# Kernel optimization log

Measured on AMD Instinct MI355X. Metric: run time of the kernel, lower is better.

## Reference

```python
import jax, jax.numpy as jnp
import numpy as np

D_MODEL = 256
NUM_HEADS = 4
D_HEAD = D_MODEL // NUM_HEADS
LN_EPS = 1e-5
NEG_INF = -1e9


def setup_inputs() -> dict:
    key = jax.random.key(0)
    ks = jax.random.split(key, 8)
    B, N = 4, 2048
    s = 1.0 / np.sqrt(D_MODEL)
    return {
        "x": jax.random.normal(ks[0], (B, N, D_MODEL), dtype=jnp.float32),
        "Wq": jax.random.normal(ks[1], (D_MODEL, D_MODEL), dtype=jnp.float32) * s,
        "Wk": jax.random.normal(ks[2], (D_MODEL, D_MODEL), dtype=jnp.float32) * s,
        "Wv": jax.random.normal(ks[3], (D_MODEL, D_MODEL), dtype=jnp.float32) * s,
        "Wo": jax.random.normal(ks[4], (D_MODEL, D_MODEL), dtype=jnp.float32) * s,
        "bo": jnp.zeros((D_MODEL,), dtype=jnp.float32),
        "gamma": jnp.ones((D_MODEL,), dtype=jnp.float32),
        "beta": jnp.zeros((D_MODEL,), dtype=jnp.float32),
        "k_neighbors": 8,
    }


def build_knn_adj(x, k):
    # x: [B, N, D]; returns symmetric 0/1 adjacency [B, N, N]
    B, N, _ = x.shape
    xn = x / jnp.maximum(jnp.linalg.norm(x, axis=-1, keepdims=True), 1e-12)
    sim = jnp.einsum('bnd,bmd->bnm', xn, xn)  # [B, N, N]
    _, idx = jax.lax.top_k(sim, k + 1)        # [B, N, k+1]
    b = jnp.arange(B)[:, None, None]
    r = jnp.arange(N)[None, :, None]
    adj = jnp.zeros((B, N, N), dtype=jnp.float32).at[b, r, idx].add(1.0)
    adj = jnp.maximum(adj, jnp.swapaxes(adj, 1, 2))
    return adj


def layer_norm(x, gamma, beta):
    mu = jnp.mean(x, axis=-1, keepdims=True)
    var = jnp.mean(jnp.square(x - mu), axis=-1, keepdims=True)
    return (x - mu) * jax.lax.rsqrt(var + LN_EPS) * gamma + beta


def reference(x, Wq, Wk, Wv, Wo, bo, gamma, beta, k_neighbors):
    B, N, D = x.shape
    adj = build_knn_adj(x, k_neighbors)  # [B, N, N]

    def split_heads(t):  # [B, N, D] -> [B, H, N, d]
        return jnp.transpose(t.reshape(B, N, NUM_HEADS, D_HEAD), (0, 2, 1, 3))

    q = split_heads(x @ Wq)
    k = split_heads(x @ Wk)
    v = split_heads(x @ Wv)

    scores = jnp.einsum('bhnd,bhmd->bhnm', q, k) / jnp.sqrt(jnp.float32(D_HEAD))
    scores = jnp.where(adj[:, None, :, :] > 0, scores, NEG_INF)
    attn = jax.nn.softmax(scores, axis=-1)  # dropout is identity at inference
    out = jnp.einsum('bhnm,bhmd->bhnd', attn, v)
    out = jnp.transpose(out, (0, 2, 1, 3)).reshape(B, N, D)
    out = out @ Wo + bo
    return layer_norm(x + out, gamma, beta)
```

## Files before the change

kernel.cpp:

```cpp
#include <hip/hip_runtime.h>
#include <hip/hip_bf16.h>
#include <math.h>

#define BATCH 4
#define N 2048
#define D 256
#define NH 4
#define DH 64
#define TOPK 9
#define NEG_BIG -1e30f

typedef __bf16 bf16;
typedef __bf16 bf16x4 __attribute__((ext_vector_type(4)));
typedef __bf16 bf16x8 __attribute__((ext_vector_type(8)));
typedef float f32x4 __attribute__((ext_vector_type(4)));

#define PK3(a,b,c) ((a) | ((b) << 2) | ((c) << 4))
#define PK6(a,b,c,d,e,f) ((a) | ((b) << 2) | ((c) << 4) | ((d) << 6) | ((e) << 8) | ((f) << 10))

#define WAITVM(Nc) __builtin_amdgcn_s_waitcnt((((Nc) & 0xf)) | (7u << 4) | (0xfu << 8) | ((((unsigned)(Nc)) >> 4) << 14))

__device__ __forceinline__ void async_cp16(const bf16* g, const bf16* l) {
  __builtin_amdgcn_global_load_lds(
      (const __attribute__((address_space(1))) void*)(uintptr_t)g,
      (__attribute__((address_space(3))) void*)(uintptr_t)l, 16, 0, 0);
}

__global__ __launch_bounds__(64) void prep_kernel(const float* __restrict__ x,
                                                  const float* __restrict__ Wq,
                                                  const float* __restrict__ Wk,
                                                  const float* __restrict__ Wv,
                                                  const float* __restrict__ Wo,
                                                  bf16* __restrict__ XsN,
                                                  bf16* __restrict__ Wt,
                                                  float* __restrict__ norms,
                                                  uint4* __restrict__ mask4) {
  int blk = blockIdx.x;
  int lane = threadIdx.x;
  if (blk < 8192) {
    float4 v = *(const float4*)(x + (size_t)blk * D + lane * 4);
    float ss = v.x * v.x + v.y * v.y + v.z * v.z + v.w * v.w;
    for (int off = 32; off; off >>= 1) ss += __shfl_down(ss, off);
    ss = __shfl(ss, 0);
    float nrm = fmaxf(sqrtf(ss), 1e-12f);
    if (lane == 0) norms[blk] = nrm;
    float sc = 1.0f / nrm;
    float xs[4] = {v.x * sc, v.y * sc, v.z * sc, v.w * sc};
    bf16* o = XsN + (size_t)blk * 512 + lane * 4;
#pragma unroll
    for (int j = 0; j < 4; ++j) {
      float xv = xs[j];
      bf16 h = (bf16)xv;
      o[j] = h;
      o[256 + j] = (bf16)(xv - (float)h);
    }
  } else if (blk < 9216) {
    int jj = blk - 8192;
    const float* W = (jj < 256) ? Wq : (jj < 512) ? Wk : (jj < 768) ? Wv : Wo;
    int j = jj & 255;
    bf16* dst = Wt + (size_t)jj * 512;
    for (int k = lane; k < 256; k += 64) {
      float w = W[(size_t)k * D + j];
      bf16 h = (bf16)w;
      dst[k] = h;
      dst[256 + k] = (bf16)(w - (float)h);
    }
  } else {
    int base = (blk - 9216) * 1024 + lane;
#pragma unroll
    for (int t = 0; t < 16; ++t)
      mask4[base + t * 64] = make_uint4(0, 0, 0, 0);
  }
}

__device__ __forceinline__ void gemm_core128x256(bf16* As, bf16* Bs,
                                                 const bf16* __restrict__ Ab,
                                                 const bf16* __restrict__ Bb,
                                                 void* __restrict__ Cvoid,
                                                 int ldc, int nsteps,
                                                 int amap, int bmap,
                                                 int row0, int col0,
                                                 int outmode, bool mirror,
                                                 const float* __restrict__ rowscale) {
  int tid = threadIdx.x;
  int lane = tid & 63;
  int wv = tid >> 6;
  int wm = (wv >> 1) * 64;
  int wn = (wv & 1) * 128;
  int fr = lane & 15;
  int G = lane >> 4;

  f32x4 acc[4][8] = {};

  auto issue = [&](int st, int buf) {
    int ch = st >> 3;
    int aoff = (((amap >> (ch * 2)) & 3) << 8) | ((st & 7) << 5);
    int boff = (((bmap >> (ch * 2)) & 3) << 8) | ((st & 7) << 5);
#pragma unroll
    for (int q = 0; q < 2; ++q) {
      int s = q * 256 + tid;
      int r = s >> 2, sl = s & 3;
      async_cp16(Ab + (size_t)r * 512 + ((sl ^ ((r >> 1) & 3)) << 3) + aoff,
                 &As[buf * 4096 + s * 8]);
    }
#pragma unroll
    for (int q = 0; q < 4; ++q) {
      int s = q * 256 + tid;
      int r = s >> 2, sl = s & 3;
      async_cp16(Bb + (size_t)r * 512 + ((sl ^ ((r >> 1) & 3)) << 3) + boff,
                 &Bs[buf * 8192 + s * 8]);
    }
  };

  issue(0, 0);
  for (int st = 0; st < nsteps; ++st) {
    int buf = st & 1;
    if (st + 1 < nsteps) {
      issue(st + 1, buf ^ 1);
      WAITVM(6);
    } else {
      WAITVM(0);
    }
    __builtin_amdgcn_s_barrier();
    bf16x8 af[4], bfr[8];
#pragma unroll
    for (int mi = 0; mi < 4; ++mi) {
      int r = wm + mi * 16 + fr;
      af[mi] = *(const bf16x8*)&As[buf * 4096 + r * 32 + ((G ^ ((r >> 1) & 3)) << 3)];
    }
#pragma unroll
    for (int nj = 0; nj < 8; ++nj) {
      int r = wn + nj * 16 + fr;
      bfr[nj] = *(const bf16x8*)&Bs[buf * 8192 + r * 32 + ((G ^ ((r >> 1) & 3)) << 3)];
    }
    __builtin_amdgcn_s_setprio(1);
#pragma unroll
    for (int mi = 0; mi < 4; ++mi)
#pragma unroll
      for (int nj = 0; nj < 8; ++nj)
        acc[mi][nj] = __builtin_amdgcn_mfma_f32_16x16x32_bf16(af[mi], bfr[nj], acc[mi][nj], 0, 0, 0);
    __builtin_amdgcn_s_setprio(0);
    __builtin_amdgcn_s_barrier();
  }

  int er = (lane >> 4) * 4;
  int ec = lane & 15;
#pragma unroll
  for (int mi = 0; mi < 4; ++mi) {
    int rb = row0 + wm + mi * 16 + er;
    float scl[4] = {1.f, 1.f, 1.f, 1.f};
    if (rowscale) {
      float4 s4 = *(const float4*)(rowscale + rb);
      scl[0] = s4.x; scl[1] = s4.y; scl[2] = s4.z; scl[3] = s4.w;
    }
#pragma unroll
    for (int nj = 0; nj < 8; ++nj) {
      int cb = col0 + wn + nj * 16 + ec;
      if (outmode == 1) {
        float* Cb = (float*)Cvoid;
#pragma unroll
        for (int reg = 0; reg < 4; ++reg)
          __builtin_nontemporal_store(acc[mi][nj][reg],
                                      &Cb[(size_t)(rb + reg) * ldc + cb]);
        if (mirror) {
          __builtin_nontemporal_store(acc[mi][nj],
                                      (f32x4*)&Cb[(size_t)cb * ldc + rb]);
        }
      } else {
        bf16* Cb = (bf16*)Cvoid;
#pragma unroll
        for (int reg = 0; reg < 4; ++reg)
          Cb[(size_t)(rb + reg) * ldc + cb] = (bf16)(acc[mi][nj][reg] * scl[reg]);
      }
    }
  }
}

__global__ __launch_bounds__(256, 2) void gemm_fused128x256_kernel(
    const bf16* __restrict__ XsN, float* __restrict__ sim,
    int amap_s, int bmap_s,
    const bf16* __restrict__ Wt, bf16* __restrict__ qkv,
    int amap_q, int bmap_q, const float* __restrict__ norms) {
  __shared__ bf16 As[2 * 128 * 32];
  __shared__ bf16 Bs[2 * 256 * 32];
  int g = blockIdx.x;
  if (g < 288) {
    int xcd = g & 7;
    int z = xcd >> 1;
    int t = (xcd & 1) * 36 + (g >> 3);
    int half = t & 1;
    int u = t >> 1;
    int by = 0;
    while (u >= 8 - by) { u -= 8 - by; ++by; }
    int bx = by + u;
    int row0 = by * 256 + half * 128;
    int col0 = bx * 256;
    gemm_core128x256(As, Bs,
                     XsN + (size_t)z * N * 512 + (size_t)row0 * 512,
                     XsN + (size_t)z * N * 512 + (size_t)col0 * 512,
                     sim + (size_t)z * N * N,
                     N, 24, amap_s, bmap_s, row0, col0,
                     1, bx != by, nullptr);
  } else {
    int t = g - 288;
    int xcd = t & 7;
    int slot = t >> 3;
    int z = xcd >> 1;
    int by = z * 16 + (xcd & 1) * 8 + slot / 3;
    int bx = slot % 3;
    gemm_core128x256(As, Bs,
                     XsN + (size_t)by * 128 * 512,
                     Wt + (size_t)bx * 256 * 512,
                     qkv, 768, 16, amap_q, bmap_q,
                     by * 128, bx * 256, 2, false, norms);
  }
}

__device__ __forceinline__ void gemm_core(bf16* As, bf16* Bs,
                                          const bf16* __restrict__ Ab,
                                          const bf16* __restrict__ Bb,
                                          void* __restrict__ Cvoid,
                                          int lda, int ldb, int ldc,
                                          int nsteps, int amap, int bmap,
                                          int row0, int col0,
                                          int outmode, bool mirror,
                                          const float* __restrict__ rowscale) {
  int tid = threadIdx.x;
  int lane = tid & 63;
  int wv = tid >> 6;
  int wm = (wv >> 1) * 64;
  int wn = (wv & 1) * 64;

  int rbase = tid >> 2;
  int gperm = (tid & 3) ^ ((rbase >> 1) & 3);
  const bf16* ga0 = Ab + (size_t)rbase * lda + gperm * 8;
  const bf16* gb0 = Bb + (size_t)rbase * ldb + gperm * 8;
  int ldsoff = tid * 8;

  int fr = lane & 15;
  int G = lane >> 4;

  f32x4 acc[4][4] = {};

  auto issue = [&](int st, int buf) {
    int ch = st >> 3;
    int aoff = (((amap >> (ch * 2)) & 3) << 8) | ((st & 7) << 5);
    int boff = (((bmap >> (ch * 2)) & 3) << 8) | ((st & 7) << 5);
#pragma unroll
    for (int q = 0; q < 2; ++q)
      async_cp16(ga0 + (size_t)q * 64 * lda + aoff, &As[buf * 4096 + ldsoff + q * 2048]);
#pragma unroll
    for (int q = 0; q < 2; ++q)
      async_cp16(gb0 + (size_t)q * 64 * ldb + boff, &Bs[buf * 4096 + ldsoff + q * 2048]);
  };

  issue(0, 0);
  for (int st = 0; st < nsteps; ++st) {
    int buf = st & 1;
    if (st + 1 < nsteps) {
      issue(st + 1, buf ^ 1);
      WAITVM(4);
    } else {
      WAITVM(0);
    }
    __builtin_amdgcn_s_barrier();
    bf16x8 af[4], bfr[4];
#pragma unroll
    for (int mi = 0; mi < 4; ++mi) {
      int r = wm + mi * 16 + fr;
      af[mi] = *(const bf16x8*)&As[buf * 4096 + r * 32 + ((G ^ ((r >> 1) & 3)) << 3)];
    }
#pragma unroll
    for (int nj = 0; nj < 4; ++nj) {
      int r = wn + nj * 16 + fr;
      bfr[nj] = *(const bf16x8*)&Bs[buf * 4096 + r * 32 + ((G ^ ((r >> 1) & 3)) << 3)];
    }
#pragma unroll
    for (int mi = 0; mi < 4; ++mi)
#pragma unroll
      for (int nj = 0; nj < 4; ++nj)
        acc[mi][nj] = __builtin_amdgcn_mfma_f32_16x16x32_bf16(af[mi], bfr[nj], acc[mi][nj], 0, 0, 0);
    __builtin_amdgcn_s_barrier();
  }

  int er = (lane >> 4) * 4;
  int ec = lane & 15;
#pragma unroll
  for (int mi = 0; mi < 4; ++mi) {
    int rb = row0 + wm + mi * 16 + er;
    float scl[4] = {1.f, 1.f, 1.f, 1.f};
    if (rowscale) {
      float4 s4 = *(const float4*)(rowscale + rb);
      scl[0] = s4.x; scl[1] = s4.y; scl[2] = s4.z; scl[3] = s4.w;
    }
#pragma unroll
    for (int nj = 0; nj < 4; ++nj) {
      int cb = col0 + wn + nj * 16 + ec;
      if (outmode == 1) {
        float* Cb = (float*)Cvoid;
#pragma unroll
        for (int reg = 0; reg < 4; ++reg)
          __builtin_nontemporal_store(acc[mi][nj][reg],
                                      &Cb[(size_t)(rb + reg) * ldc + cb]);
        if (mirror) {
#pragma unroll
          for (int reg = 0; reg < 4; ++reg)
            __builtin_nontemporal_store(acc[mi][nj][reg],
                                        &Cb[(size_t)cb * ldc + rb + reg]);
        }
      } else {
        bf16* Cb = (bf16*)Cvoid;
#pragma unroll
        for (int reg = 0; reg < 4; ++reg)
          Cb[(size_t)(rb + reg) * ldc + cb] = (bf16)(acc[mi][nj][reg] * scl[reg]);
      }
    }
  }
}

__global__ __launch_bounds__(256, 4) void gemm_sim_kernel(const bf16* __restrict__ XsN,
                                                          float* __restrict__ sim,
                                                          int amap, int bmap) {
  __shared__ bf16 As[2 * 128 * 32];
  __shared__ bf16 Bs[2 * 128 * 32];
  int g = blockIdx.x;
  int xcd = g & 7;
  int slot = g >> 3;
  int z = xcd >> 1;
  int t = (xcd & 1) * 68 + slot;
  int by = 0;
  while (t >= 16 - by) { t -= 16 - by; ++by; }
  int bx = by + t;
  gemm_core(As, Bs,
            XsN + (size_t)z * N * 512 + (size_t)by * 128 * 512,
            XsN + (size_t)z * N * 512 + (size_t)bx * 128 * 512,
            sim + (size_t)z * N * N,
            512, 512, N, 24, amap, bmap, by * 128, bx * 128,
            1, bx != by, nullptr);
}

__global__ __launch_bounds__(256, 4) void gemm_qkv_kernel(const bf16* __restrict__ XsN,
                                                          const bf16* __restrict__ Wt,
                                                          bf16* __restrict__ qkv,
                                                          int amap, int bmap,
                                                          const float* __restrict__ norms) {
  __shared__ bf16 As[2 * 128 * 32];
  __shared__ bf16 Bs[2 * 128 * 32];
  gemm_core(As, Bs,
            XsN + (size_t)blockIdx.y * 128 * 512,
            Wt + (size_t)blockIdx.x * 128 * 512,
            qkv, 512, 512, 768, 16, amap, bmap,
            blockIdx.y * 128, blockIdx.x * 128, 2, false, norms);
}

__global__ __launch_bounds__(64) void topk_adj_kernel(const float* __restrict__ sim,
                                                      unsigned* __restrict__ mask) {
  int row = blockIdx.x;
  int lane = threadIdx.x;
  int b = row >> 11, r = row & 2047;
  const float* srow = sim + (size_t)row * N;
  float v[32];
#pragma unroll
  for (int it = 0; it < 8; ++it) {
    float4 q = *(const float4*)(srow + it * 256 + lane * 4);
    v[it * 4 + 0] = q.x; v[it * 4 + 1] = q.y;
    v[it * 4 + 2] = q.z; v[it * 4 + 3] = q.w;
  }
  unsigned removed = 0;
  for (int rs = 0; rs < TOPK; ++rs) {
    float m = -3e38f;
    int mi = 0;
#pragma unroll
    for (int i = 0; i < 32; ++i) {
      float vv = ((removed >> i) & 1u) ? -3e38f : v[i];
      if (vv > m) { m = vv; mi = i; }
    }
    int gidx = ((mi >> 2) << 8) + lane * 4 + (mi & 3);
    for (int off = 32; off; off >>= 1) {
      float om = __shfl_down(m, off);
      int og = __shfl_down(gidx, off);
      if (om > m || (om == m && og < gidx)) { m = om; gidx = og; }
    }
    gidx = __shfl(gidx, 0);
    if (((gidx >> 2) & 63) == lane)
      removed |= 1u << (((gidx >> 8) << 2) | (gidx & 3));
    if (lane == 0) {
      atomicOr(&mask[(size_t)row * 64 + (gidx >> 5)], 1u << (gidx & 31));
      atomicOr(&mask[(((size_t)b << 11) + gidx) * 64 + (r >> 5)], 1u << (r & 31));
    }
  }
}

__global__ __launch_bounds__(256) void attn_kernel(const bf16* __restrict__ qkv,
                                                   const unsigned* __restrict__ mask,
                                                   bf16* __restrict__ aos) {
  __shared__ float sq[4][256];
  __shared__ unsigned short nbr[4][2048];
  __shared__ int s_nn[4];
  int wv = threadIdx.x >> 6;
  int lane = threadIdx.x & 63;
  int g = blockIdx.x;
  int xcd = g & 7;
  int b = xcd >> 1;
  int tile = (xcd & 1) * 256 + (g >> 3);
  int bn = b * N + tile * 4 + wv;
  if (lane == 0) s_nn[wv] = 0;
  {
    bf16x4 qv = *(const bf16x4*)(qkv + (size_t)bn * 768 + lane * 4);
#pragma unroll
    for (int j = 0; j < 4; ++j) sq[wv][lane * 4 + j] = (float)qv[j];
  }
  __syncthreads();
  unsigned bits = mask[(size_t)bn * (N / 32) + lane];
  while (bits) {
    int bit = __ffs(bits) - 1;
    bits &= bits - 1;
    int p = atomicAdd(&s_nn[wv], 1);
    nbr[wv][p] = (unsigned short)(lane * 32 + bit);
  }
  __syncthreads();
  int nn = s_nn[wv];
  const bf16* base = qkv + (size_t)b * N * 768;
  float acc[4] = {0.f, 0.f, 0.f, 0.f};

  auto score4 = [&](int j, float* s) {
    const bf16* kr = base + (size_t)j * 768 + 256;
#pragma unroll
    for (int h = 0; h < 4; ++h) {
      float a = 0.f;
#pragma unroll
      for (int c = 0; c < DH; c += 8) {
        bf16x8 kk = *(const bf16x8*)(kr + h * DH + c);
#pragma unroll
        for (int t = 0; t < 8; ++t) a += sq[wv][h * DH + c + t] * (float)kk[t];
      }
      s[h] = a * 0.125f;
    }
  };

  if (nn <= 64) {
    float s[4] = {NEG_BIG, NEG_BIG, NEG_BIG, NEG_BIG};
    if (lane < nn) score4(nbr[wv][lane], s);
    float w[4], l[4];
#pragma unroll
    for (int h = 0; h < 4; ++h) {
      float m = s[h];
      for (int off = 32; off; off >>= 1) m = fmaxf(m, __shfl_down(m, off));
      m = __shfl(m, 0);
      float e = (lane < nn) ? __expf(s[h] - m) : 0.f;
      float ls = e;
      for (int off = 32; off; off >>= 1) ls += __shfl_down(ls, off);
      l[h] = __shfl(ls, 0);
      w[h] = e;
    }
    int i = 0;
    for (; i + 4 <= nn; i += 4) {
      int j0 = nbr[wv][i + 0], j1 = nbr[wv][i + 1];
      int j2 = nbr[wv][i + 2], j3 = nbr[wv][i + 3];
      const bf16* p0 = base + (size_t)j0 * 768 + 512;
      const bf16* p1 = base + (size_t)j1 * 768 + 512;
      const bf16* p2 = base + (size_t)j2 * 768 + 512;
      const bf16* p3 = base + (size_t)j3 * 768 + 512;
#pragma unroll
      for (int h = 0; h < 4; ++h) {
        acc[h] += __shfl(w[h], i + 0) * (float)p0[h * DH + lane] +
                  __shfl(w[h], i + 1) * (float)p1[h * DH + lane] +
                  __shfl(w[h], i + 2) * (float)p2[h * DH + lane] +
                  __shfl(w[h], i + 3) * (float)p3[h * DH + lane];
      }
    }
    for (; i < nn; ++i) {
      const bf16* p0 = base + (size_t)nbr[wv][i] * 768 + 512;
#pragma unroll
      for (int h = 0; h < 4; ++h) acc[h] += __shfl(w[h], i) * (float)p0[h * DH + lane];
    }
#pragma unroll
    for (int h = 0; h < 4; ++h) acc[h] /= l[h];
  } else {
    float m[4] = {NEG_BIG, NEG_BIG, NEG_BIG, NEG_BIG};
    for (int i0 = 0; i0 < nn; i0 += 64) {
      float s[4] = {NEG_BIG, NEG_BIG, NEG_BIG, NEG_BIG};
      if (i0 + lane < nn) score4(nbr[wv][i0 + lane], s);
#pragma unroll
      for (int h = 0; h < 4; ++h) m[h] = fmaxf(m[h], s[h]);
    }
#pragma unroll
    for (int h = 0; h < 4; ++h) {
      for (int off = 32; off; off >>= 1) m[h] = fmaxf(m[h], __shfl_down(m[h], off));
      m[h] = __shfl(m[h], 0);
    }
    float l[4] = {0.f, 0.f, 0.f, 0.f};
    for (int i0 = 0; i0 < nn; i0 += 64) {
      float s[4] = {NEG_BIG, NEG_BIG, NEG_BIG, NEG_BIG};
      if (i0 + lane < nn) score4(nbr[wv][i0 + lane], s);
      float e[4];
#pragma unroll
      for (int h = 0; h < 4; ++h) {
        e[h] = (i0 + lane < nn) ? __expf(s[h] - m[h]) : 0.f;
        float ls = e[h];
        for (int off = 32; off; off >>= 1) ls += __shfl_down(ls, off);
        l[h] += __shfl(ls, 0);
      }
      int lim = min(64, nn - i0);
      for (int ii = 0; ii < lim; ++ii) {
        const bf16* p0 = base + (size_t)nbr[wv][i0 + ii] * 768 + 512;
#pragma unroll
        for (int h = 0; h < 4; ++h) acc[h] += __shfl(e[h], ii) * (float)p0[h * DH + lane];
      }
    }
#pragma unroll
    for (int h = 0; h < 4; ++h) acc[h] /= l[h];
  }
#pragma unroll
  for (int h = 0; h < 4; ++h) {
    float a = acc[h];
    bf16 hi = (bf16)a;
    aos[(size_t)bn * 512 + h * DH + lane] = hi;
    aos[(size_t)bn * 512 + 256 + h * DH + lane] = (bf16)(a - (float)hi);
  }
}

__global__ __launch_bounds__(256) void projln_kernel(const bf16* __restrict__ A,
                                                     const bf16* __restrict__ Bw,
                                                     const float* __restrict__ x,
                                                     const float* __restrict__ bo,
                                                     const float* __restrict__ gamma,
                                                     const float* __restrict__ beta,
                                                     float* __restrict__ out) {
  __shared__ bf16 As[2 * 32 * 32];
  __shared__ bf16 Bs[2 * 256 * 32];
  __shared__ float rsum[32][4];
  __shared__ float rsq[32][4];
  int tid = threadIdx.x;
  int lane = tid & 63;
  int wv = tid >> 6;
  int wn = wv * 64;
  int row0 = blockIdx.x * 32;

  int rt = tid >> 2;
  int ra = tid >> 2;
  int gpa = (tid & 3) ^ ((ra >> 1) & 3);
  const bf16* ga0 = A + (size_t)(row0 + ra) * 512 + gpa * 8;

  int fr = lane & 15;
  int G = lane >> 4;

  f32x4 acc[2][4] = {};

  auto issue = [&](int st, int buf) {
    int aoff = ((st >> 3) << 8) | ((st & 7) << 5);
    int boff = (st & 7) << 5;
    if (tid < 128)
      async_cp16(ga0 + aoff, &As[buf * 1024 + tid * 8]);
#pragma unroll
    for (int q = 0; q < 4; ++q) {
      int rb = q * 64 + rt;
      int gpb = (tid & 3) ^ ((rb >> 1) & 3);
      async_cp16(Bw + (size_t)rb * 512 + gpb * 8 + boff,
                 &Bs[buf * 8192 + (q * 256 + tid) * 8]);
    }
  };

  issue(0, 0);
  for (int st = 0; st < 16; ++st) {
    int buf = st & 1;
    if (st + 1 < 16) {
      issue(st + 1, buf ^ 1);
      WAITVM(4);
    } else {
      WAITVM(0);
    }
    __builtin_amdgcn_s_barrier();
    bf16x8 af[2], bfr[4];
#pragma unroll
    for (int mi = 0; mi < 2; ++mi) {
      int r = mi * 16 + fr;
      af[mi] = *(const bf16x8*)&As[buf * 1024 + r * 32 + ((G ^ ((r >> 1) & 3)) << 3)];
    }
#pragma unroll
    for (int nj = 0; nj < 4; ++nj) {
      int r = wn + nj * 16 + fr;
      bfr[nj] = *(const bf16x8*)&Bs[buf * 8192 + r * 32 + ((G ^ ((r >> 1) & 3)) << 3)];
    }
#pragma unroll
    for (int mi = 0; mi < 2; ++mi)
#pragma unroll
      for (int nj = 0; nj < 4; ++nj)
        acc[mi][nj] = __builtin_amdgcn_mfma_f32_16x16x32_bf16(af[mi], bfr[nj], acc[mi][nj], 0, 0, 0);
    __builtin_amdgcn_s_barrier();
  }

  int er = (lane >> 4) * 4;
  int ec = lane & 15;
  float bo_c[4], ga_c[4], be_c[4];
#pragma unroll
  for (int nj = 0; nj < 4; ++nj) {
    int c = wn + nj * 16 + ec;
    bo_c[nj] = bo[c]; ga_c[nj] = gamma[c]; be_c[nj] = beta[c];
  }
#pragma unroll
  for (int mi = 0; mi < 2; ++mi)
#pragma unroll
    for (int reg = 0; reg < 4; ++reg) {
      int rloc = mi * 16 + er + reg;
      const float* xr = x + (size_t)(row0 + rloc) * D;
      float su = 0.f, s2 = 0.f;
#pragma unroll
      for (int nj = 0; nj < 4; ++nj) {
        float u = acc[mi][nj][reg] + bo_c[nj] + xr[wn + nj * 16 + ec];
        su += u; s2 += u * u;
      }
#pragma unroll
      for (int m = 1; m <= 8; m <<= 1) {
        su += __shfl_xor(su, m);
        s2 += __shfl_xor(s2, m);
      }
      if (ec == 0) { rsum[rloc][wv] = su; rsq[rloc][wv] = s2; }
    }
  __syncthreads();
#pragma unroll
  for (int mi = 0; mi < 2; ++mi)
#pragma unroll
    for (int reg = 0; reg < 4; ++reg) {
      int rloc = mi * 16 + er + reg;
      float s = rsum[rloc][0] + rsum[rloc][1] + rsum[rloc][2] + rsum[rloc][3];
      float q2 = rsq[rloc][0] + rsq[rloc][1] + rsq[rloc][2] + rsq[rloc][3];
      float mean = s * (1.0f / D);
      float var = q2 * (1.0f / D) - mean * mean;
      float rstd = rsqrtf(var + 1e-5f);
      const float* xr = x + (size_t)(row0 + rloc) * D;
      float* orow = out + (size_t)(row0 + rloc) * D;
#pragma unroll
      for (int nj = 0; nj < 4; ++nj) {
        float u = acc[mi][nj][reg] + bo_c[nj] + xr[wn + nj * 16 + ec];
        orow[wn + nj * 16 + ec] = (u - mean) * rstd * ga_c[nj] + be_c[nj];
      }
    }
}

extern "C" void kernel_launch(void* const* d_in, const int* in_sizes, int n_in,
                              void* d_out, int out_size, void* d_ws, size_t ws_size,
                              hipStream_t stream) {
  const float* x     = (const float*)d_in[0];
  const float* Wq    = (const float*)d_in[1];
  const float* Wk    = (const float*)d_in[2];
  const float* Wv    = (const float*)d_in[3];
  const float* Wo    = (const float*)d_in[4];
  const float* bo    = (const float*)d_in[5];
  const float* gamma = (const float*)d_in[6];
  const float* beta  = (const float*)d_in[7];
  float* out = (float*)d_out;

  char* ws = (char*)d_ws;
  bf16* XsN      = (bf16*)(ws);
  float* sim     = (float*)(ws + 12582912);
  float* norms   = (float*)(ws + 79691776);
  unsigned* mask = (unsigned*)(ws + 79986688);
  bf16* Wt       = (bf16*)(ws + 82083840);

  bool big = ws_size >= (size_t)125000000;
  bf16* qkv = (bf16*)(ws + (big ? 83132416 : 12582912));
  bf16* aos = (bf16*)(ws + (big ? 95715328 : 37748736));

  const int AMAP_SIM = PK6(0, 0, 1, 0, 0, 0);
  const int BMAP_SIM = PK6(0, 1, 0, 0, 0, 0);
  const int AMAP_2T  = PK3(0, 1, 0);
  const int BMAP_2T  = PK3(0, 0, 1);

  prep_kernel<<<9344, 64, 0, stream>>>(x, Wq, Wk, Wv, Wo, XsN, Wt, norms,
                                       (uint4*)mask);

  if (big) {
    gemm_fused128x256_kernel<<<480, 256, 0, stream>>>(
        XsN, sim, AMAP_SIM, BMAP_SIM, Wt, qkv, AMAP_2T, BMAP_2T, norms);
    topk_adj_kernel<<<BATCH * N, 64, 0, stream>>>(sim, mask);
  } else {
    gemm_sim_kernel<<<544, 256, 0, stream>>>(XsN, sim, AMAP_SIM, BMAP_SIM);
    topk_adj_kernel<<<BATCH * N, 64, 0, stream>>>(sim, mask);
    gemm_qkv_kernel<<<dim3(6, 64), 256, 0, stream>>>(XsN, Wt, qkv,
                                                     AMAP_2T, BMAP_2T, norms);
  }

  attn_kernel<<<(BATCH * N) / 4, 256, 0, stream>>>(qkv, mask, aos);

  projln_kernel<<<256, 256, 0, stream>>>(aos, Wt + (size_t)768 * 512,
                                         x, bo, gamma, beta, out);
}
```

Baseline: 187.8 us.

## Fuse per-tile top-k candidate selection into similarity GEMM epilogue

```diff
diff --git a/kernel.cpp b/kernel.cpp
--- a/kernel.cpp
+++ b/kernel.cpp
@@ -143,30 +143,92 @@
     __builtin_amdgcn_s_barrier();
   }
 
-  int er = (lane >> 4) * 4;
-  int ec = lane & 15;
-#pragma unroll
-  for (int mi = 0; mi < 4; ++mi) {
-    int rb = row0 + wm + mi * 16 + er;
-    float scl[4] = {1.f, 1.f, 1.f, 1.f};
-    if (rowscale) {
-      float4 s4 = *(const float4*)(rowscale + rb);
-      scl[0] = s4.x; scl[1] = s4.y; scl[2] = s4.z; scl[3] = s4.w;
-    }
-#pragma unroll
-    for (int nj = 0; nj < 8; ++nj) {
-      int cb = col0 + wn + nj * 16 + ec;
-      if (outmode == 1) {
-        float* Cb = (float*)Cvoid;
-#pragma unroll
-        for (int reg = 0; reg < 4; ++reg)
-          __builtin_nontemporal_store(acc[mi][nj][reg],
-                                      &Cb[(size_t)(rb + reg) * ldc + cb]);
-        if (mirror) {
-          __builtin_nontemporal_store(acc[mi][nj],
-                                      (f32x4*)&Cb[(size_t)cb * ldc + rb]);
+  int ecl = lane & 15;
+  int erg = lane >> 4;
+
+  if (outmode == 1) {
+    uint2* cand = (uint2*)Cvoid;
+#pragma unroll
+    for (int g4 = 0; g4 < 2; ++g4) {
+      int colbase = col0 + wn + g4 * 64;
+      int slot = colbase >> 6;
+#pragma unroll
+      for (int mi = 0; mi < 4; ++mi)
+#pragma unroll
+        for (int reg = 0; reg < 4; ++reg) {
+          int row = row0 + wm + mi * 16 + erg * 4 + reg;
+          float v0 = acc[mi][g4 * 4 + 0][reg];
+          float v1 = acc[mi][g4 * 4 + 1][reg];
+          float v2 = acc[mi][g4 * 4 + 2][reg];
+          float v3 = acc[mi][g4 * 4 + 3][reg];
+          uint2* dst = cand + ((size_t)row * 32 + slot) * 9;
+          unsigned rm = 0;
+          for (int k = 0; k < TOPK; ++k) {
+            float t0 = (rm & 1u) ? -3e38f : v0;
+            float t1 = (rm & 2u) ? -3e38f : v1;
+            float t2 = (rm & 4u) ? -3e38f : v2;
+            float t3 = (rm & 8u) ? -3e38f : v3;
+            float bv = t0; int bi = colbase + ecl;
+            if (t1 > bv) { bv = t1; bi = colbase + 16 + ecl; }
+            if (t2 > bv) { bv = t2; bi = colbase + 32 + ecl; }
+            if (t3 > bv) { bv = t3; bi = colbase + 48 + ecl; }
+#pragma unroll
+            for (int m = 1; m <= 8; m <<= 1) {
+              float ov = __shfl_xor(bv, m);
+              int oi = __shfl_xor(bi, m);
+              if (ov > bv || (ov == bv && oi < bi)) { bv = ov; bi = oi; }
+            }
+            int pos = bi - colbase;
+            if ((pos & 15) == ecl) rm |= 1u << (pos >> 4);
+            if (ecl == k) dst[k] = make_uint2(__float_as_uint(bv), (unsigned)bi);
+          }
         }
-      } else {
+    }
+    if (mirror) {
+      int rowbase = row0 + wm;
+      int slot = rowbase >> 6;
+#pragma unroll
+      for (int nj = 0; nj < 8; ++nj) {
+        int c = col0 + wn + nj * 16 + ecl;
+        uint2* dst = cand + ((size_t)c * 32 + slot) * 9;
+        unsigned rm = 0;
+        for (int k = 0; k < TOPK; ++k) {
+          float bv = -3e38f; int bi = 0x7fffffff;
+#pragma unroll
+          for (int mi = 0; mi < 4; ++mi)
+#pragma unroll
+            for (int reg = 0; reg < 4; ++reg) {
+              int bit = mi * 4 + reg;
+              float vv = ((rm >> bit) & 1u) ? -3e38f : acc[mi][nj][reg];
+              int ri = rowbase + mi * 16 + erg * 4 + reg;
+              if (vv > bv || (vv == bv && ri < bi)) { bv = vv; bi = ri; }
+            }
+#pragma unroll
+          for (int m = 16; m <= 32; m <<= 1) {
+            float ov = __shfl_xor(bv, m);
+            int oi = __shfl_xor(bi, m);
+            if (ov > bv || (ov == bv && oi < bi)) { bv = ov; bi = oi; }
+          }
+          int pos = bi - rowbase;
+          if (((pos >> 2) & 3) == erg)
+            rm |= 1u << (((pos >> 4) << 2) | (pos & 3));
+          if (erg == 0) dst[k] = make_uint2(__float_as_uint(bv), (unsigned)bi);
+        }
+      }
+    }
+  } else {
+    int er = erg * 4;
+#pragma unroll
+    for (int mi = 0; mi < 4; ++mi) {
+      int rb = row0 + wm + mi * 16 + er;
+      float scl[4] = {1.f, 1.f, 1.f, 1.f};
+      if (rowscale) {
+        float4 s4 = *(const float4*)(rowscale + rb);
+        scl[0] = s4.x; scl[1] = s4.y; scl[2] = s4.z; scl[3] = s4.w;
+      }
+#pragma unroll
+      for (int nj = 0; nj < 8; ++nj) {
+        int cb = col0 + wn + nj * 16 + ecl;
         bf16* Cb = (bf16*)Cvoid;
 #pragma unroll
         for (int reg = 0; reg < 4; ++reg)
@@ -177,7 +239,7 @@
 }
 
 __global__ __launch_bounds__(256, 2) void gemm_fused128x256_kernel(
-    const bf16* __restrict__ XsN, float* __restrict__ sim,
+    const bf16* __restrict__ XsN, uint2* __restrict__ cand,
     int amap_s, int bmap_s,
     const bf16* __restrict__ Wt, bf16* __restrict__ qkv,
     int amap_q, int bmap_q, const float* __restrict__ norms) {
@@ -198,8 +260,8 @@
     gemm_core128x256(As, Bs,
                      XsN + (size_t)z * N * 512 + (size_t)row0 * 512,
                      XsN + (size_t)z * N * 512 + (size_t)col0 * 512,
-                     sim + (size_t)z * N * N,
-                     N, 24, amap_s, bmap_s, row0, col0,
+                     cand + (size_t)z * N * 288,
+                     0, 24, amap_s, bmap_s, row0, col0,
                      1, bx != by, nullptr);
   } else {
     int t = g - 288;
@@ -213,6 +275,48 @@
                      Wt + (size_t)bx * 256 * 512,
                      qkv, 768, 16, amap_q, bmap_q,
                      by * 128, bx * 256, 2, false, norms);
+  }
+}
+
+__global__ __launch_bounds__(64) void topk_merge_kernel(const uint2* __restrict__ cand,
+                                                        unsigned* __restrict__ mask) {
+  int row = blockIdx.x;
+  int lane = threadIdx.x;
+  int b = row >> 11, r = row & 2047;
+  const uint2* crow = cand + (size_t)row * 288;
+  float v[5]; int ci[5];
+#pragma unroll
+  for (int t = 0; t < 4; ++t) {
+    uint2 p = crow[lane + 64 * t];
+    v[t] = __uint_as_float(p.x); ci[t] = (int)p.y;
+  }
+  if (lane < 32) {
+    uint2 p = crow[256 + lane];
+    v[4] = __uint_as_float(p.x); ci[4] = (int)p.y;
+  } else {
+    v[4] = -3e38f; ci[4] = 0x7fffffff;
+  }
+  unsigned rm = 0;
+  for (int k = 0; k < TOPK; ++k) {
+    float bv = -3e38f; int bi = 0x7fffffff;
+#pragma unroll
+    for (int t = 0; t < 5; ++t) {
+      float vv = ((rm >> t) & 1u) ? -3e38f : v[t];
+      if (vv > bv || (vv == bv && ci[t] < bi)) { bv = vv; bi = ci[t]; }
+    }
+#pragma unroll
+    for (int off = 1; off < 64; off <<= 1) {
+      float ov = __shfl_xor(bv, off);
+      int oi = __shfl_xor(bi, off);
+      if (ov > bv || (ov == bv && oi < bi)) { bv = ov; bi = oi; }
+    }
+#pragma unroll
+    for (int t = 0; t < 5; ++t)
+      if (ci[t] == bi) rm |= 1u << t;
+    if (lane == 0) {
+      atomicOr(&mask[(size_t)row * 64 + (bi >> 5)], 1u << (bi & 31));
+      atomicOr(&mask[(((size_t)b << 11) + bi) * 64 + (r >> 5)], 1u << (r & 31));
+    }
   }
 }
 
@@ -654,6 +758,7 @@
   char* ws = (char*)d_ws;
   bf16* XsN      = (bf16*)(ws);
   float* sim     = (float*)(ws + 12582912);
+  uint2* cand    = (uint2*)(ws + 12582912);
   float* norms   = (float*)(ws + 79691776);
   unsigned* mask = (unsigned*)(ws + 79986688);
   bf16* Wt       = (bf16*)(ws + 82083840);
@@ -672,8 +777,8 @@
 
   if (big) {
     gemm_fused128x256_kernel<<<480, 256, 0, stream>>>(
-        XsN, sim, AMAP_SIM, BMAP_SIM, Wt, qkv, AMAP_2T, BMAP_2T, norms);
-    topk_adj_kernel<<<BATCH * N, 64, 0, stream>>>(sim, mask);
+        XsN, cand, AMAP_SIM, BMAP_SIM, Wt, qkv, AMAP_2T, BMAP_2T, norms);
+    topk_merge_kernel<<<BATCH * N, 64, 0, stream>>>(cand, mask);
   } else {
     gemm_sim_kernel<<<544, 256, 0, stream>>>(XsN, sim, AMAP_SIM, BMAP_SIM);
     topk_adj_kernel<<<BATCH * N, 64, 0, stream>>>(sim, mask);
```

Measured after the change: 359.6 us. 91.5% more time.
